# Kernel tuning notes

Hardware: AMD Instinct MI355X
Metric: run time of the kernel (lower is better)

## Reference

```python
import jax, jax.numpy as jnp
import numpy as np

B, C, T, D = 32, 1024, 64, 64
F_OUT = 128      # out_channels
S_DIM = 64       # stage_dim
N_STG = 5        # num_stages
H_MLP = 64       # hidden of stage_mlp


def setup_inputs() -> dict:
    key = jax.random.key(0)
    ks = jax.random.split(key, 16)
    sc = 0.05
    return {
        "x": jax.random.normal(ks[0], (B, C, T, D), dtype=jnp.float32),
        "A_init": jax.random.uniform(ks[1], (C, C), dtype=jnp.float32),
        "W_proj": jax.random.normal(ks[2], (F_OUT, D), dtype=jnp.float32) * sc,
        "b_proj": jnp.zeros((F_OUT,), dtype=jnp.float32),
        "W_s1": jax.random.normal(ks[3], (H_MLP, D), dtype=jnp.float32) * sc,
        "b_s1": jnp.zeros((H_MLP,), dtype=jnp.float32),
        "W_s2": jax.random.normal(ks[4], (N_STG, H_MLP), dtype=jnp.float32) * sc,
        "b_s2": jnp.zeros((N_STG,), dtype=jnp.float32),
        "W_c1": jax.random.normal(ks[5], (S_DIM, N_STG), dtype=jnp.float32) * sc,
        "b_c1": jnp.zeros((S_DIM,), dtype=jnp.float32),
        "W_c2": jax.random.normal(ks[6], (S_DIM, S_DIM), dtype=jnp.float32) * sc,
        "b_c2": jnp.zeros((S_DIM,), dtype=jnp.float32),
        "att": jax.random.normal(ks[7], (2 * F_OUT + S_DIM,), dtype=jnp.float32) * sc,
        "lam": jnp.array([0.5], dtype=jnp.float32),
    }


def reference(x, A_init, W_proj, b_proj, W_s1, b_s1, W_s2, b_s2,
              W_c1, b_c1, W_c2, b_c2, att, lam):
    F = W_proj.shape[0]
    x_red = jnp.mean(x, axis=2)                               # (B,C,D)
    Z = x_red @ W_proj.T + b_proj                             # (B,C,F)
    x_glob = jnp.mean(x_red, axis=1)                          # (B,D)
    s = jax.nn.softmax(
        jax.nn.relu(x_glob @ W_s1.T + b_s1) @ W_s2.T + b_s2, axis=-1)  # (B,num_stages)
    c = jax.nn.relu(s @ W_c1.T + b_c1) @ W_c2.T + b_c2        # (B,stage_dim)
    # Split att_weight: sum over concat([Z_i, Z_j, c]) * att == dot-per-part
    a_i, a_j, a_c = att[:F], att[F:2 * F], att[2 * F:]
    e = ((Z @ a_i)[:, :, None]            # (B,C,1) broadcast over j
         + (Z @ a_j)[:, None, :]          # (B,1,C) broadcast over i
         + (c @ a_c)[:, None, None])      # (B,1,1)
    e = jax.nn.leaky_relu(e, negative_slope=0.2)              # (B,C,C)
    eps = 1e-8
    e_tilde = e + lam[0] * jnp.log(A_init + eps)[None, :, :]
    alpha = jax.nn.softmax(e_tilde, axis=-1)                  # (B,C,C)
    h = alpha @ Z                                             # (B,C,F)
    return h, s
```

## Files before the change

kernel.cpp:

```cpp
#include <hip/hip_runtime.h>
#include <cstddef>
#include <math.h>


typedef __attribute__((ext_vector_type(8))) short bf16x8;
typedef __attribute__((ext_vector_type(4))) float f32x4;

__device__ inline unsigned f2bf(float f) {
  unsigned u = __float_as_uint(f);
  return (u + 0x7FFFu + ((u >> 16) & 1u)) >> 16;
}

#define LOGA_OFF 0u
#define EI_OFF   1048576u
#define EJ_OFF   1081344u
#define PXG_OFF  1114112u
#define ZK_OFF   1179648u

__global__ __launch_bounds__(256) void k_fuse1(
    const float4* __restrict__ X4, const float* __restrict__ A,
    const float* __restrict__ lam, const float* __restrict__ W,
    const float* __restrict__ bproj, const float* __restrict__ att,
    uint4* __restrict__ Zk, float* __restrict__ ei, float* __restrict__ ej,
    float4* __restrict__ pXG4, float* __restrict__ llogA) {
  int tid = threadIdx.x;
  int bk = blockIdx.x;
  if (bk >= 1024) {
    float l = lam[0];
    int base = (bk - 1024) * 1024 + tid;
#pragma unroll
    for (int k = 0; k < 4; ++k)
      llogA[base + k * 256] = l * __logf(A[base + k * 256] + 1e-8f);
    return;
  }
  __shared__ float Wl[64 * 129];
  __shared__ float4 xr4[32 * 16];
  int rb = bk * 32;

#pragma unroll
  for (int k = 0; k < 32; ++k) {
    int g = k * 256 + tid;
    Wl[(g & 63) * 129 + (g >> 6)] = W[g];
  }

  {
    int row = tid >> 3, g = tid & 7;
    const float4* xbase = X4 + ((size_t)(rb + row)) * 1024 + g;
    float4 a0 = make_float4(0.f, 0.f, 0.f, 0.f), a1 = a0;
#pragma unroll
    for (int k = 0; k < 128; k += 2) {
      float4 v0 = xbase[k * 8];
      float4 v1 = xbase[k * 8 + 8];
      a0.x += v0.x; a0.y += v0.y; a0.z += v0.z; a0.w += v0.w;
      a1.x += v1.x; a1.y += v1.y; a1.z += v1.z; a1.w += v1.w;
    }
    const float inv = 1.0f / 64.0f;
    a0.x *= inv; a0.y *= inv; a0.z *= inv; a0.w *= inv;
    a1.x *= inv; a1.y *= inv; a1.z *= inv; a1.w *= inv;
    xr4[row * 16 + g] = a0;
    xr4[row * 16 + g + 8] = a1;
  }
  __syncthreads();

  if (tid < 16) {
    float4 p = make_float4(0.f, 0.f, 0.f, 0.f);
#pragma unroll
    for (int r = 0; r < 32; ++r) {
      float4 v = xr4[r * 16 + tid];
      p.x += v.x; p.y += v.y; p.z += v.z; p.w += v.w;
    }
    pXG4[bk * 16 + tid] = p;
  }

  int f = tid & 127, rg = tid >> 7;
  float wreg[64];
#pragma unroll
  for (int d = 0; d < 64; ++d) wreg[d] = Wl[d * 129 + f];
  float bias = bproj[f];
  float acc[16];
#pragma unroll
  for (int r = 0; r < 16; ++r) acc[r] = bias;
#pragma unroll
  for (int r = 0; r < 16; ++r) {
    int row = rg * 16 + r;
#pragma unroll
    for (int dq = 0; dq < 16; ++dq) {
      float4 xv = xr4[row * 16 + dq];
      acc[r] = fmaf(wreg[dq * 4 + 0], xv.x, acc[r]);
      acc[r] = fmaf(wreg[dq * 4 + 1], xv.y, acc[r]);
      acc[r] = fmaf(wreg[dq * 4 + 2], xv.z, acc[r]);
      acc[r] = fmaf(wreg[dq * 4 + 3], xv.w, acc[r]);
    }
  }
  int b = rb >> 10;
  int cbase = (rb & 1023) + rg * 16;
#pragma unroll
  for (int k2 = 0; k2 < 2; ++k2) {
    unsigned w0 = f2bf(acc[k2 * 8 + 0]) | (f2bf(acc[k2 * 8 + 1]) << 16);
    unsigned w1 = f2bf(acc[k2 * 8 + 2]) | (f2bf(acc[k2 * 8 + 3]) << 16);
    unsigned w2 = f2bf(acc[k2 * 8 + 4]) | (f2bf(acc[k2 * 8 + 5]) << 16);
    unsigned w3 = f2bf(acc[k2 * 8 + 6]) | (f2bf(acc[k2 * 8 + 7]) << 16);
    size_t chunk = ((size_t)b * 128 + ((cbase >> 3) + k2)) * 128 + f;
    Zk[chunk] = make_uint4(w0, w1, w2, w3);
  }
  __syncthreads();
  float* Zl = Wl;
#pragma unroll
  for (int r = 0; r < 16; ++r)
    Zl[(rg * 16 + r) * 130 + f] = acc[r];
  __syncthreads();
  int row = tid >> 3, g = tid & 7;
  float si = 0.f, sj = 0.f;
#pragma unroll
  for (int u = 0; u < 16; ++u) {
    float z = Zl[row * 130 + g * 16 + u];
    si = fmaf(z, att[g * 16 + u], si);
    sj = fmaf(z, att[128 + g * 16 + u], sj);
  }
  si += __shfl_xor(si, 1); sj += __shfl_xor(sj, 1);
  si += __shfl_xor(si, 2); sj += __shfl_xor(sj, 2);
  si += __shfl_xor(si, 4); sj += __shfl_xor(sj, 4);
  if (g == 0) { ei[rb + row] = si; ej[rb + row] = sj; }
}

__global__ __launch_bounds__(64) void k_main(const uint4* __restrict__ Zk,
    const float* __restrict__ llogA, const float* __restrict__ ei,
    const float* __restrict__ ej, const float* __restrict__ pXG,
    const float* __restrict__ Ws1, const float* __restrict__ bs1,
    const float* __restrict__ Ws2, const float* __restrict__ bs2,
    const float* __restrict__ Wc1, const float* __restrict__ bc1,
    const float* __restrict__ Wc2, const float* __restrict__ bc2,
    const float* __restrict__ att,
    float* __restrict__ hout, float* __restrict__ sout) {
  int bid = blockIdx.x;
  int b = ((bid & 7) << 2) | ((bid >> 3) & 3);
  int rowgrp = bid >> 5;
  int i0 = rowgrp * 16;
  int lane = threadIdx.x;
  int lg = lane >> 4, ln = lane & 15;

  float ecb;
  {
    float xg = 0.f;
    const float* pb = pXG + (size_t)b * 32 * 64;
#pragma unroll 8
    for (int p = 0; p < 32; ++p) xg += pb[p * 64 + lane];
    xg *= (1.0f / 1024.0f);
    const float* w1 = Ws1 + lane * 64;
    float h = bs1[lane];
#pragma unroll 16
    for (int d = 0; d < 64; ++d) h = fmaf(__shfl(xg, d), w1[d], h);
    h = fmaxf(h, 0.f);
    int ln5 = lane < 5 ? lane : 4;
    const float* w2 = Ws2 + ln5 * 64;
    float l = bs2[ln5];
#pragma unroll 16
    for (int k = 0; k < 64; ++k) l = fmaf(__shfl(h, k), w2[k], l);
    float s0 = __shfl(l, 0), s1 = __shfl(l, 1), s2 = __shfl(l, 2),
          s3 = __shfl(l, 3), s4 = __shfl(l, 4);
    float m = fmaxf(fmaxf(fmaxf(s0, s1), fmaxf(s2, s3)), s4);
    float e0 = __expf(s0 - m), e1 = __expf(s1 - m), e2 = __expf(s2 - m),
          e3 = __expf(s3 - m), e4 = __expf(s4 - m);
    float inv = 1.0f / (e0 + e1 + e2 + e3 + e4);
    s0 = e0 * inv; s1 = e1 * inv; s2 = e2 * inv; s3 = e3 * inv; s4 = e4 * inv;
    if (rowgrp == 0 && lane == 0) {
      sout[b * 5 + 0] = s0; sout[b * 5 + 1] = s1; sout[b * 5 + 2] = s2;
      sout[b * 5 + 3] = s3; sout[b * 5 + 4] = s4;
    }
    const float* wc1 = Wc1 + lane * 5;
    float cv = bc1[lane];
    cv = fmaf(s0, wc1[0], cv); cv = fmaf(s1, wc1[1], cv);
    cv = fmaf(s2, wc1[2], cv); cv = fmaf(s3, wc1[3], cv);
    cv = fmaf(s4, wc1[4], cv);
    cv = fmaxf(cv, 0.f);
    const float* wc2 = Wc2 + lane * 64;
    float c2 = bc2[lane];
#pragma unroll 16
    for (int k = 0; k < 64; ++k) c2 = fmaf(__shfl(cv, k), wc2[k], c2);
    float v = c2 * att[256 + lane];
#pragma unroll
    for (int o = 32; o; o >>= 1) v += __shfl_xor(v, o);
    ecb = v;
  }

  int i_gl = i0 + ln;
  float eir = ei[b * 1024 + i_gl];
  const float4* lrow4 = (const float4*)(llogA + (size_t)i_gl * 1024);
  const float4* ejr4  = (const float4*)(ej + b * 1024);
  const uint4*  ZkB   = Zk + (size_t)b * 128 * 128;

  float m_run = -1e30f, s_run = 0.0f;
  f32x4 acc[8];
#pragma unroll
  for (int q = 0; q < 8; ++q) { f32x4 z = {0.f, 0.f, 0.f, 0.f}; acc[q] = z; }

  for (int jt = 0; jt < 16; ++jt) {
    int j0 = jt * 64;
    uint4 bz[2][8];
#pragma unroll
    for (int ks = 0; ks < 2; ++ks)
#pragma unroll
      for (int fb = 0; fb < 8; ++fb)
        bz[ks][fb] = ZkB[(size_t)((j0 >> 3) + ks * 4 + lg) * 128 + fb * 16 + ln];
    float tv[16];
    float tm = -1e30f;
#pragma unroll
    for (int ks = 0; ks < 2; ++ks) {
      int jb = (j0 + ks * 32 + lg * 8) >> 2;
      float4 e0 = ejr4[jb], e1 = ejr4[jb + 1];
      float4 l0 = lrow4[jb], l1 = lrow4[jb + 1];
      float eq[8] = {e0.x, e0.y, e0.z, e0.w, e1.x, e1.y, e1.z, e1.w};
      float lq[8] = {l0.x, l0.y, l0.z, l0.w, l1.x, l1.y, l1.z, l1.w};
#pragma unroll
      for (int u = 0; u < 8; ++u) {
        float t = eir + eq[u] + ecb;
        t = t > 0.0f ? t : 0.2f * t;
        t += lq[u];
        tv[ks * 8 + u] = t;
        tm = fmaxf(tm, t);
      }
    }
    tm = fmaxf(tm, __shfl_xor(tm, 16));
    tm = fmaxf(tm, __shfl_xor(tm, 32));
    float newm = fmaxf(m_run, tm);
    float scale = __expf(m_run - newm);
    float ts = 0.0f;
    unsigned pw[8];
#pragma unroll
    for (int q = 0; q < 8; ++q) {
      float p0 = __expf(tv[2 * q] - newm);
      float p1 = __expf(tv[2 * q + 1] - newm);
      ts += p0 + p1;
      pw[q] = f2bf(p0) | (f2bf(p1) << 16);
    }
    ts += __shfl_xor(ts, 16);
    ts += __shfl_xor(ts, 32);
    s_run = s_run * scale + ts;
    m_run = newm;
#pragma unroll
    for (int q = 0; q < 8; ++q) acc[q] *= scale;
    union { unsigned u[4]; bf16x8 v; } c0, c1;
#pragma unroll
    for (int q = 0; q < 4; ++q) { c0.u[q] = pw[q]; c1.u[q] = pw[4 + q]; }
#pragma unroll
    for (int fb = 0; fb < 8; ++fb)
      acc[fb] = __builtin_amdgcn_mfma_f32_16x16x32_bf16(c0.v, *(bf16x8*)&bz[0][fb], acc[fb], 0, 0, 0);
#pragma unroll
    for (int fb = 0; fb < 8; ++fb)
      acc[fb] = __builtin_amdgcn_mfma_f32_16x16x32_bf16(c1.v, *(bf16x8*)&bz[1][fb], acc[fb], 0, 0, 0);
  }

  float invs = 1.0f / s_run;
  float inv_m[4];
#pragma unroll
  for (int r = 0; r < 4; ++r) inv_m[r] = __shfl(invs, lg * 4 + r);
  float* hb = hout + ((size_t)b * 1024 + i0 + lg * 4) * 128 + ln;
#pragma unroll
  for (int fb = 0; fb < 8; ++fb) {
#pragma unroll
    for (int r = 0; r < 4; ++r)
      hb[(size_t)r * 128 + fb * 16] = acc[fb][r] * inv_m[r];
  }
}

extern "C" void kernel_launch(void* const* d_in, const int* in_sizes, int n_in,
                              void* d_out, int out_size, void* d_ws, size_t ws_size,
                              hipStream_t stream) {
  const float* x     = (const float*)d_in[0];
  const float* Ainit = (const float*)d_in[1];
  const float* Wproj = (const float*)d_in[2];
  const float* bproj = (const float*)d_in[3];
  const float* Ws1   = (const float*)d_in[4];
  const float* bs1   = (const float*)d_in[5];
  const float* Ws2   = (const float*)d_in[6];
  const float* bs2   = (const float*)d_in[7];
  const float* Wc1   = (const float*)d_in[8];
  const float* bc1   = (const float*)d_in[9];
  const float* Wc2   = (const float*)d_in[10];
  const float* bc2   = (const float*)d_in[11];
  const float* att   = (const float*)d_in[12];
  const float* lam   = (const float*)d_in[13];

  float* ws    = (float*)d_ws;
  float* llogA = ws + LOGA_OFF;
  float* ei    = ws + EI_OFF;
  float* ej    = ws + EJ_OFF;
  float* pXG   = ws + PXG_OFF;
  uint4* Zk    = (uint4*)(ws + ZK_OFF);

  float* hout = (float*)d_out;
  float* sout = hout + (size_t)32 * 1024 * 128;

  hipLaunchKernelGGL(k_fuse1, dim3(2048), dim3(256), 0, stream,
                     (const float4*)x, Ainit, lam, Wproj, bproj, att,
                     Zk, ei, ej, (float4*)pXG, llogA);
  hipLaunchKernelGGL(k_main,  dim3(2048), dim3(64),  0, stream,
                     Zk, llogA, ei, ej, pXG,
                     Ws1, bs1, Ws2, bs2, Wc1, bc1, Wc2, bc2, att,
                     hout, sout);
}
```

Before: 180.6 us.

## Split k_main feature columns across waves, share stage MLP, skip redundant rescale

k_main now runs 256-thread blocks in which four waves cover two row groups, each wave handling half of the 128 output features. The stage MLP is computed once per block by wave 0 and shared through shared memory, so it is no longer repeated in every 64-thread block. The online softmax skips rescaling the accumulators when the running max does not change. k_fuse1 reads projection weights straight from global memory as float4 instead of transposing them through shared memory, which removes a barrier. In exchange, the per-row softmax exp work is now duplicated across the two feature-half waves, and the kernel adds a block barrier plus a divergent branch.

Result: slower. 207.4 us (+14.9%).

```diff
diff --git a/kernel.cpp b/kernel.cpp
--- a/kernel.cpp
+++ b/kernel.cpp
@@ -33,15 +33,9 @@
       llogA[base + k * 256] = l * __logf(A[base + k * 256] + 1e-8f);
     return;
   }
-  __shared__ float Wl[64 * 129];
   __shared__ float4 xr4[32 * 16];
+  __shared__ float Zl[32 * 130];
   int rb = bk * 32;
-
-#pragma unroll
-  for (int k = 0; k < 32; ++k) {
-    int g = k * 256 + tid;
-    Wl[(g & 63) * 129 + (g >> 6)] = W[g];
-  }
 
   {
     int row = tid >> 3, g = tid & 7;
@@ -74,8 +68,15 @@
 
   int f = tid & 127, rg = tid >> 7;
   float wreg[64];
-#pragma unroll
-  for (int d = 0; d < 64; ++d) wreg[d] = Wl[d * 129 + f];
+  {
+    const float4* Wf = (const float4*)(W + f * 64);
+#pragma unroll
+    for (int q = 0; q < 16; ++q) {
+      float4 w = Wf[q];
+      wreg[q * 4 + 0] = w.x; wreg[q * 4 + 1] = w.y;
+      wreg[q * 4 + 2] = w.z; wreg[q * 4 + 3] = w.w;
+    }
+  }
   float bias = bproj[f];
   float acc[16];
 #pragma unroll
@@ -103,8 +104,6 @@
     size_t chunk = ((size_t)b * 128 + ((cbase >> 3) + k2)) * 128 + f;
     Zk[chunk] = make_uint4(w0, w1, w2, w3);
   }
-  __syncthreads();
-  float* Zl = Wl;
 #pragma unroll
   for (int r = 0; r < 16; ++r)
     Zl[(rg * 16 + r) * 130 + f] = acc[r];
@@ -123,7 +122,7 @@
   if (g == 0) { ei[rb + row] = si; ej[rb + row] = sj; }
 }
 
-__global__ __launch_bounds__(64) void k_main(const uint4* __restrict__ Zk,
+__global__ __launch_bounds__(256) void k_main(const uint4* __restrict__ Zk,
     const float* __restrict__ llogA, const float* __restrict__ ei,
     const float* __restrict__ ej, const float* __restrict__ pXG,
     const float* __restrict__ Ws1, const float* __restrict__ bs1,
@@ -132,15 +131,18 @@
     const float* __restrict__ Wc2, const float* __restrict__ bc2,
     const float* __restrict__ att,
     float* __restrict__ hout, float* __restrict__ sout) {
+  __shared__ float ec_s;
   int bid = blockIdx.x;
   int b = ((bid & 7) << 2) | ((bid >> 3) & 3);
-  int rowgrp = bid >> 5;
+  int rgpair = bid >> 5;
+  int tid = threadIdx.x;
+  int wave = tid >> 6, lane = tid & 63;
+  int rowgrp = rgpair * 2 + (wave >> 1);
+  int fbase = (wave & 1) * 4;
   int i0 = rowgrp * 16;
-  int lane = threadIdx.x;
   int lg = lane >> 4, ln = lane & 15;
 
-  float ecb;
-  {
+  if (wave == 0) {
     float xg = 0.f;
     const float* pb = pXG + (size_t)b * 32 * 64;
 #pragma unroll 8
@@ -163,7 +165,7 @@
           e3 = __expf(s3 - m), e4 = __expf(s4 - m);
     float inv = 1.0f / (e0 + e1 + e2 + e3 + e4);
     s0 = e0 * inv; s1 = e1 * inv; s2 = e2 * inv; s3 = e3 * inv; s4 = e4 * inv;
-    if (rowgrp == 0 && lane == 0) {
+    if (rgpair == 0 && lane == 0) {
       sout[b * 5 + 0] = s0; sout[b * 5 + 1] = s1; sout[b * 5 + 2] = s2;
       sout[b * 5 + 3] = s3; sout[b * 5 + 4] = s4;
     }
@@ -180,8 +182,10 @@
     float v = c2 * att[256 + lane];
 #pragma unroll
     for (int o = 32; o; o >>= 1) v += __shfl_xor(v, o);
-    ecb = v;
-  }
+    if (lane == 0) ec_s = v;
+  }
+  __syncthreads();
+  float ecb = ec_s;
 
   int i_gl = i0 + ln;
   float eir = ei[b * 1024 + i_gl];
@@ -190,18 +194,19 @@
   const uint4*  ZkB   = Zk + (size_t)b * 128 * 128;
 
   float m_run = -1e30f, s_run = 0.0f;
-  f32x4 acc[8];
-#pragma unroll
-  for (int q = 0; q < 8; ++q) { f32x4 z = {0.f, 0.f, 0.f, 0.f}; acc[q] = z; }
+  f32x4 acc[4];
+#pragma unroll
+  for (int q = 0; q < 4; ++q) { f32x4 z = {0.f, 0.f, 0.f, 0.f}; acc[q] = z; }
 
   for (int jt = 0; jt < 16; ++jt) {
     int j0 = jt * 64;
-    uint4 bz[2][8];
+    uint4 bz[2][4];
 #pragma unroll
     for (int ks = 0; ks < 2; ++ks)
 #pragma unroll
-      for (int fb = 0; fb < 8; ++fb)
-        bz[ks][fb] = ZkB[(size_t)((j0 >> 3) + ks * 4 + lg) * 128 + fb * 16 + ln];
+      for (int fb = 0; fb < 4; ++fb)
+        bz[ks][fb] = ZkB[(size_t)((j0 >> 3) + ks * 4 + lg) * 128
+                         + (fbase + fb) * 16 + ln];
     float tv[16];
     float tm = -1e30f;
 #pragma unroll
@@ -223,30 +228,33 @@
     tm = fmaxf(tm, __shfl_xor(tm, 16));
     tm = fmaxf(tm, __shfl_xor(tm, 32));
     float newm = fmaxf(m_run, tm);
-    float scale = __expf(m_run - newm);
+    if (!__all(tm <= m_run)) {
+      float scale = __expf(m_run - newm);
+      s_run *= scale;
+#pragma unroll
+      for (int q = 0; q < 4; ++q) acc[q] *= scale;
+      m_run = newm;
+    }
     float ts = 0.0f;
     unsigned pw[8];
 #pragma unroll
     for (int q = 0; q < 8; ++q) {
-      float p0 = __expf(tv[2 * q] - newm);
-      float p1 = __expf(tv[2 * q + 1] - newm);
+      float p0 = __expf(tv[2 * q] - m_run);
+      float p1 = __expf(tv[2 * q + 1] - m_run);
       ts += p0 + p1;
       pw[q] = f2bf(p0) | (f2bf(p1) << 16);
     }
     ts += __shfl_xor(ts, 16);
     ts += __shfl_xor(ts, 32);
-    s_run = s_run * scale + ts;
-    m_run = newm;
-#pragma unroll
-    for (int q = 0; q < 8; ++q) acc[q] *= scale;
+    s_run += ts;
     union { unsigned u[4]; bf16x8 v; } c0, c1;
 #pragma unroll
     for (int q = 0; q < 4; ++q) { c0.u[q] = pw[q]; c1.u[q] = pw[4 + q]; }
 #pragma unroll
-    for (int fb = 0; fb < 8; ++fb)
+    for (int fb = 0; fb < 4; ++fb)
       acc[fb] = __builtin_amdgcn_mfma_f32_16x16x32_bf16(c0.v, *(bf16x8*)&bz[0][fb], acc[fb], 0, 0, 0);
 #pragma unroll
-    for (int fb = 0; fb < 8; ++fb)
+    for (int fb = 0; fb < 4; ++fb)
       acc[fb] = __builtin_amdgcn_mfma_f32_16x16x32_bf16(c1.v, *(bf16x8*)&bz[1][fb], acc[fb], 0, 0, 0);
   }
 
@@ -254,9 +262,9 @@
   float inv_m[4];
 #pragma unroll
   for (int r = 0; r < 4; ++r) inv_m[r] = __shfl(invs, lg * 4 + r);
-  float* hb = hout + ((size_t)b * 1024 + i0 + lg * 4) * 128 + ln;
-#pragma unroll
-  for (int fb = 0; fb < 8; ++fb) {
+  float* hb = hout + ((size_t)b * 1024 + i0 + lg * 4) * 128 + fbase * 16 + ln;
+#pragma unroll
+  for (int fb = 0; fb < 4; ++fb) {
 #pragma unroll
     for (int r = 0; r < 4; ++r)
       hb[(size_t)r * 128 + fb * 16] = acc[fb][r] * inv_m[r];
@@ -294,7 +302,7 @@
   hipLaunchKernelGGL(k_fuse1, dim3(2048), dim3(256), 0, stream,
                      (const float4*)x, Ainit, lam, Wproj, bproj, att,
                      Zk, ei, ej, (float4*)pXG, llogA);
-  hipLaunchKernelGGL(k_main,  dim3(2048), dim3(64),  0, stream,
+  hipLaunchKernelGGL(k_main,  dim3(1024), dim3(256), 0, stream,
                      Zk, llogA, ei, ej, pXG,
                      Ws1, bs1, Ws2, bs2, Wc1, bc1, Wc2, bc2, att,
                      hout, sout);
```

## Double-buffer Z and logA tile loads and stage ej in shared memory

Applied to the files above, without the earlier changes.

The main attention kernel's j-tile loop now prefetches the next tile's Z fragments and logA row values into a second register buffer while the current tile is processed. This lets global-load latency overlap the softmax and MFMA work. The per-batch ej vector is also copied into LDS once at kernel start instead of being read from global memory every tile. The cost is roughly double the register footprint for the Z buffers, which may reduce occupancy or cause spills, plus one extra barrier.

New measurement: 183.7 us. No clear change (+1.8%).

```diff
diff --git a/kernel.cpp b/kernel.cpp
--- a/kernel.cpp
+++ b/kernel.cpp
@@ -132,12 +132,18 @@
     const float* __restrict__ Wc2, const float* __restrict__ bc2,
     const float* __restrict__ att,
     float* __restrict__ hout, float* __restrict__ sout) {
+  __shared__ float4 ejs4[256];
   int bid = blockIdx.x;
   int b = ((bid & 7) << 2) | ((bid >> 3) & 3);
   int rowgrp = bid >> 5;
   int i0 = rowgrp * 16;
   int lane = threadIdx.x;
   int lg = lane >> 4, ln = lane & 15;
+
+  const float4* ej4 = (const float4*)(ej + b * 1024);
+#pragma unroll
+  for (int k = 0; k < 4; ++k) ejs4[k * 64 + lane] = ej4[k * 64 + lane];
+  __syncthreads();
 
   float ecb;
   {
@@ -186,7 +192,6 @@
   int i_gl = i0 + ln;
   float eir = ei[b * 1024 + i_gl];
   const float4* lrow4 = (const float4*)(llogA + (size_t)i_gl * 1024);
-  const float4* ejr4  = (const float4*)(ej + b * 1024);
   const uint4*  ZkB   = Zk + (size_t)b * 128 * 128;
 
   float m_run = -1e30f, s_run = 0.0f;
@@ -194,61 +199,72 @@
 #pragma unroll
   for (int q = 0; q < 8; ++q) { f32x4 z = {0.f, 0.f, 0.f, 0.f}; acc[q] = z; }
 
-  for (int jt = 0; jt < 16; ++jt) {
-    int j0 = jt * 64;
-    uint4 bz[2][8];
-#pragma unroll
-    for (int ks = 0; ks < 2; ++ks)
-#pragma unroll
-      for (int fb = 0; fb < 8; ++fb)
-        bz[ks][fb] = ZkB[(size_t)((j0 >> 3) + ks * 4 + lg) * 128 + fb * 16 + ln];
-    float tv[16];
-    float tm = -1e30f;
-#pragma unroll
-    for (int ks = 0; ks < 2; ++ks) {
-      int jb = (j0 + ks * 32 + lg * 8) >> 2;
-      float4 e0 = ejr4[jb], e1 = ejr4[jb + 1];
-      float4 l0 = lrow4[jb], l1 = lrow4[jb + 1];
-      float eq[8] = {e0.x, e0.y, e0.z, e0.w, e1.x, e1.y, e1.z, e1.w};
-      float lq[8] = {l0.x, l0.y, l0.z, l0.w, l1.x, l1.y, l1.z, l1.w};
-#pragma unroll
-      for (int u = 0; u < 8; ++u) {
-        float t = eir + eq[u] + ecb;
-        t = t > 0.0f ? t : 0.2f * t;
-        t += lq[u];
-        tv[ks * 8 + u] = t;
-        tm = fmaxf(tm, t);
-      }
-    }
-    tm = fmaxf(tm, __shfl_xor(tm, 16));
-    tm = fmaxf(tm, __shfl_xor(tm, 32));
-    float newm = fmaxf(m_run, tm);
-    float scale = __expf(m_run - newm);
-    float ts = 0.0f;
-    unsigned pw[8];
-#pragma unroll
-    for (int q = 0; q < 8; ++q) {
-      float p0 = __expf(tv[2 * q] - newm);
-      float p1 = __expf(tv[2 * q + 1] - newm);
-      ts += p0 + p1;
-      pw[q] = f2bf(p0) | (f2bf(p1) << 16);
-    }
-    ts += __shfl_xor(ts, 16);
-    ts += __shfl_xor(ts, 32);
-    s_run = s_run * scale + ts;
-    m_run = newm;
-#pragma unroll
-    for (int q = 0; q < 8; ++q) acc[q] *= scale;
-    union { unsigned u[4]; bf16x8 v; } c0, c1;
-#pragma unroll
-    for (int q = 0; q < 4; ++q) { c0.u[q] = pw[q]; c1.u[q] = pw[4 + q]; }
-#pragma unroll
-    for (int fb = 0; fb < 8; ++fb)
-      acc[fb] = __builtin_amdgcn_mfma_f32_16x16x32_bf16(c0.v, *(bf16x8*)&bz[0][fb], acc[fb], 0, 0, 0);
-#pragma unroll
-    for (int fb = 0; fb < 8; ++fb)
-      acc[fb] = __builtin_amdgcn_mfma_f32_16x16x32_bf16(c1.v, *(bf16x8*)&bz[1][fb], acc[fb], 0, 0, 0);
-  }
+#define LOAD_BZ(buf, jt_) do { int j0_ = (jt_) * 64;                          \
+  _Pragma("unroll") for (int ks = 0; ks < 2; ++ks)                            \
+    _Pragma("unroll") for (int fb = 0; fb < 8; ++fb)                          \
+      buf[ks][fb] = ZkB[(size_t)((j0_ >> 3) + ks * 4 + lg) * 128              \
+                        + fb * 16 + ln];                                      \
+} while (0)
+
+#define LOAD_LA(buf, jt_) do { int j0_ = (jt_) * 64;                          \
+  _Pragma("unroll") for (int ks = 0; ks < 2; ++ks) {                          \
+    int jb = (j0_ + ks * 32 + lg * 8) >> 2;                                   \
+    buf[ks][0] = lrow4[jb]; buf[ks][1] = lrow4[jb + 1]; }                     \
+} while (0)
+
+#define PROCESS(jt_, bz, la) do { int j0_ = (jt_) * 64;                       \
+  float tv[16]; float tm = -1e30f;                                            \
+  _Pragma("unroll") for (int ks = 0; ks < 2; ++ks) {                          \
+    int jb = (j0_ + ks * 32 + lg * 8) >> 2;                                   \
+    float4 e0 = ejs4[jb], e1 = ejs4[jb + 1];                                  \
+    float4 l0 = la[ks][0], l1 = la[ks][1];                                    \
+    float eq[8] = {e0.x, e0.y, e0.z, e0.w, e1.x, e1.y, e1.z, e1.w};           \
+    float lq[8] = {l0.x, l0.y, l0.z, l0.w, l1.x, l1.y, l1.z, l1.w};           \
+    _Pragma("unroll") for (int u = 0; u < 8; ++u) {                           \
+      float t = eir + eq[u] + ecb;                                            \
+      t = t > 0.0f ? t : 0.2f * t;                                            \
+      t += lq[u];                                                             \
+      tv[ks * 8 + u] = t; tm = fmaxf(tm, t); } }                              \
+  tm = fmaxf(tm, __shfl_xor(tm, 16));                                         \
+  tm = fmaxf(tm, __shfl_xor(tm, 32));                                         \
+  float newm = fmaxf(m_run, tm);                                              \
+  float scale = __expf(m_run - newm);                                         \
+  float ts = 0.0f; unsigned pw[8];                                            \
+  _Pragma("unroll") for (int q = 0; q < 8; ++q) {                             \
+    float p0 = __expf(tv[2 * q] - newm);                                      \
+    float p1 = __expf(tv[2 * q + 1] - newm);                                  \
+    ts += p0 + p1; pw[q] = f2bf(p0) | (f2bf(p1) << 16); }                     \
+  ts += __shfl_xor(ts, 16); ts += __shfl_xor(ts, 32);                         \
+  s_run = s_run * scale + ts; m_run = newm;                                   \
+  _Pragma("unroll") for (int q = 0; q < 8; ++q) acc[q] *= scale;              \
+  union { unsigned u[4]; bf16x8 v; } c0, c1;                                  \
+  _Pragma("unroll") for (int q = 0; q < 4; ++q) {                             \
+    c0.u[q] = pw[q]; c1.u[q] = pw[4 + q]; }                                   \
+  _Pragma("unroll") for (int fb = 0; fb < 8; ++fb)                            \
+    acc[fb] = __builtin_amdgcn_mfma_f32_16x16x32_bf16(                        \
+        c0.v, *(bf16x8*)&bz[0][fb], acc[fb], 0, 0, 0);                        \
+  _Pragma("unroll") for (int fb = 0; fb < 8; ++fb)                            \
+    acc[fb] = __builtin_amdgcn_mfma_f32_16x16x32_bf16(                        \
+        c1.v, *(bf16x8*)&bz[1][fb], acc[fb], 0, 0, 0);                        \
+} while (0)
+
+  uint4 bzA[2][8], bzB[2][8];
+  float4 laA[2][2], laB[2][2];
+  LOAD_BZ(bzA, 0);
+  LOAD_LA(laA, 0);
+  for (int jt = 0; jt < 16; jt += 2) {
+    LOAD_BZ(bzB, jt + 1);
+    LOAD_LA(laB, jt + 1);
+    PROCESS(jt, bzA, laA);
+    if (jt + 2 < 16) {
+      LOAD_BZ(bzA, jt + 2);
+      LOAD_LA(laA, jt + 2);
+    }
+    PROCESS(jt + 1, bzB, laB);
+  }
+#undef LOAD_BZ
+#undef LOAD_LA
+#undef PROCESS
 
   float invs = 1.0f / s_run;
   float inv_m[4];
```

## Split stage MLP into own kernel and halve feature columns per attention block

Applied to the files above, without the earlier changes.

Moves the per-batch stage MLP and softmax, previously recomputed by every attention block, into a small separate kernel that writes the scalar c·a_c term to workspace. The main attention kernel now launches twice as many single-wave blocks, each covering half of the 128 output features. This reduces register pressure and raises occupancy (launch bounds 64,4), and the second Z tile load is moved after the logit computation. It also adds s_setprio around the MFMA block. The cost is that each block recomputes the exp/softmax statistics for its rows twice and there is an extra kernel launch.

New measurement: 196.3 us. 1.09x slower.

```diff
diff --git a/kernel.cpp b/kernel.cpp
--- a/kernel.cpp
+++ b/kernel.cpp
@@ -16,6 +16,7 @@
 #define EJ_OFF   1081344u
 #define PXG_OFF  1114112u
 #define ZK_OFF   1179648u
+#define EC_OFF   3276800u
 
 __global__ __launch_bounds__(256) void k_fuse1(
     const float4* __restrict__ X4, const float* __restrict__ A,
@@ -123,85 +124,88 @@
   if (g == 0) { ei[rb + row] = si; ej[rb + row] = sj; }
 }
 
-__global__ __launch_bounds__(64) void k_main(const uint4* __restrict__ Zk,
-    const float* __restrict__ llogA, const float* __restrict__ ei,
-    const float* __restrict__ ej, const float* __restrict__ pXG,
+__global__ __launch_bounds__(64) void k_ec(const float* __restrict__ pXG,
     const float* __restrict__ Ws1, const float* __restrict__ bs1,
     const float* __restrict__ Ws2, const float* __restrict__ bs2,
     const float* __restrict__ Wc1, const float* __restrict__ bc1,
     const float* __restrict__ Wc2, const float* __restrict__ bc2,
     const float* __restrict__ att,
-    float* __restrict__ hout, float* __restrict__ sout) {
+    float* __restrict__ sout, float* __restrict__ ec) {
+  int b = blockIdx.x;
+  int lane = threadIdx.x;
+  float xg = 0.f;
+  const float* pb = pXG + (size_t)b * 32 * 64;
+#pragma unroll 8
+  for (int p = 0; p < 32; ++p) xg += pb[p * 64 + lane];
+  xg *= (1.0f / 1024.0f);
+  const float* w1 = Ws1 + lane * 64;
+  float h = bs1[lane];
+#pragma unroll 16
+  for (int d = 0; d < 64; ++d) h = fmaf(__shfl(xg, d), w1[d], h);
+  h = fmaxf(h, 0.f);
+  int ln5 = lane < 5 ? lane : 4;
+  const float* w2 = Ws2 + ln5 * 64;
+  float l = bs2[ln5];
+#pragma unroll 16
+  for (int k = 0; k < 64; ++k) l = fmaf(__shfl(h, k), w2[k], l);
+  float s0 = __shfl(l, 0), s1 = __shfl(l, 1), s2 = __shfl(l, 2),
+        s3 = __shfl(l, 3), s4 = __shfl(l, 4);
+  float m = fmaxf(fmaxf(fmaxf(s0, s1), fmaxf(s2, s3)), s4);
+  float e0 = __expf(s0 - m), e1 = __expf(s1 - m), e2 = __expf(s2 - m),
+        e3 = __expf(s3 - m), e4 = __expf(s4 - m);
+  float inv = 1.0f / (e0 + e1 + e2 + e3 + e4);
+  s0 = e0 * inv; s1 = e1 * inv; s2 = e2 * inv; s3 = e3 * inv; s4 = e4 * inv;
+  if (lane == 0) {
+    sout[b * 5 + 0] = s0; sout[b * 5 + 1] = s1; sout[b * 5 + 2] = s2;
+    sout[b * 5 + 3] = s3; sout[b * 5 + 4] = s4;
+  }
+  const float* wc1 = Wc1 + lane * 5;
+  float cv = bc1[lane];
+  cv = fmaf(s0, wc1[0], cv); cv = fmaf(s1, wc1[1], cv);
+  cv = fmaf(s2, wc1[2], cv); cv = fmaf(s3, wc1[3], cv);
+  cv = fmaf(s4, wc1[4], cv);
+  cv = fmaxf(cv, 0.f);
+  const float* wc2 = Wc2 + lane * 64;
+  float c2 = bc2[lane];
+#pragma unroll 16
+  for (int k = 0; k < 64; ++k) c2 = fmaf(__shfl(cv, k), wc2[k], c2);
+  float v = c2 * att[256 + lane];
+#pragma unroll
+  for (int o = 32; o; o >>= 1) v += __shfl_xor(v, o);
+  if (lane == 0) ec[b] = v;
+}
+
+__global__ __launch_bounds__(64, 4) void k_main(const uint4* __restrict__ Zk,
+    const float* __restrict__ llogA, const float* __restrict__ ei,
+    const float* __restrict__ ej, const float* __restrict__ ecw,
+    float* __restrict__ hout) {
   int bid = blockIdx.x;
   int b = ((bid & 7) << 2) | ((bid >> 3) & 3);
-  int rowgrp = bid >> 5;
+  int r = bid >> 5;
+  int rowgrp = r >> 1;
+  int fbase = (r & 1) * 4;
   int i0 = rowgrp * 16;
   int lane = threadIdx.x;
   int lg = lane >> 4, ln = lane & 15;
 
-  float ecb;
-  {
-    float xg = 0.f;
-    const float* pb = pXG + (size_t)b * 32 * 64;
-#pragma unroll 8
-    for (int p = 0; p < 32; ++p) xg += pb[p * 64 + lane];
-    xg *= (1.0f / 1024.0f);
-    const float* w1 = Ws1 + lane * 64;
-    float h = bs1[lane];
-#pragma unroll 16
-    for (int d = 0; d < 64; ++d) h = fmaf(__shfl(xg, d), w1[d], h);
-    h = fmaxf(h, 0.f);
-    int ln5 = lane < 5 ? lane : 4;
-    const float* w2 = Ws2 + ln5 * 64;
-    float l = bs2[ln5];
-#pragma unroll 16
-    for (int k = 0; k < 64; ++k) l = fmaf(__shfl(h, k), w2[k], l);
-    float s0 = __shfl(l, 0), s1 = __shfl(l, 1), s2 = __shfl(l, 2),
-          s3 = __shfl(l, 3), s4 = __shfl(l, 4);
-    float m = fmaxf(fmaxf(fmaxf(s0, s1), fmaxf(s2, s3)), s4);
-    float e0 = __expf(s0 - m), e1 = __expf(s1 - m), e2 = __expf(s2 - m),
-          e3 = __expf(s3 - m), e4 = __expf(s4 - m);
-    float inv = 1.0f / (e0 + e1 + e2 + e3 + e4);
-    s0 = e0 * inv; s1 = e1 * inv; s2 = e2 * inv; s3 = e3 * inv; s4 = e4 * inv;
-    if (rowgrp == 0 && lane == 0) {
-      sout[b * 5 + 0] = s0; sout[b * 5 + 1] = s1; sout[b * 5 + 2] = s2;
-      sout[b * 5 + 3] = s3; sout[b * 5 + 4] = s4;
-    }
-    const float* wc1 = Wc1 + lane * 5;
-    float cv = bc1[lane];
-    cv = fmaf(s0, wc1[0], cv); cv = fmaf(s1, wc1[1], cv);
-    cv = fmaf(s2, wc1[2], cv); cv = fmaf(s3, wc1[3], cv);
-    cv = fmaf(s4, wc1[4], cv);
-    cv = fmaxf(cv, 0.f);
-    const float* wc2 = Wc2 + lane * 64;
-    float c2 = bc2[lane];
-#pragma unroll 16
-    for (int k = 0; k < 64; ++k) c2 = fmaf(__shfl(cv, k), wc2[k], c2);
-    float v = c2 * att[256 + lane];
-#pragma unroll
-    for (int o = 32; o; o >>= 1) v += __shfl_xor(v, o);
-    ecb = v;
-  }
-
   int i_gl = i0 + ln;
   float eir = ei[b * 1024 + i_gl];
+  float ecb = ecw[b];
   const float4* lrow4 = (const float4*)(llogA + (size_t)i_gl * 1024);
   const float4* ejr4  = (const float4*)(ej + b * 1024);
   const uint4*  ZkB   = Zk + (size_t)b * 128 * 128;
 
   float m_run = -1e30f, s_run = 0.0f;
-  f32x4 acc[8];
-#pragma unroll
-  for (int q = 0; q < 8; ++q) { f32x4 z = {0.f, 0.f, 0.f, 0.f}; acc[q] = z; }
+  f32x4 acc[4];
+#pragma unroll
+  for (int q = 0; q < 4; ++q) { f32x4 z = {0.f, 0.f, 0.f, 0.f}; acc[q] = z; }
 
   for (int jt = 0; jt < 16; ++jt) {
     int j0 = jt * 64;
-    uint4 bz[2][8];
-#pragma unroll
-    for (int ks = 0; ks < 2; ++ks)
-#pragma unroll
-      for (int fb = 0; fb < 8; ++fb)
-        bz[ks][fb] = ZkB[(size_t)((j0 >> 3) + ks * 4 + lg) * 128 + fb * 16 + ln];
+    uint4 bz0[4];
+#pragma unroll
+    for (int fb = 0; fb < 4; ++fb)
+      bz0[fb] = ZkB[(size_t)((j0 >> 3) + lg) * 128 + (fbase + fb) * 16 + ln];
     float tv[16];
     float tm = -1e30f;
 #pragma unroll
@@ -220,6 +224,10 @@
         tm = fmaxf(tm, t);
       }
     }
+    uint4 bz1[4];
+#pragma unroll
+    for (int fb = 0; fb < 4; ++fb)
+      bz1[fb] = ZkB[(size_t)((j0 >> 3) + 4 + lg) * 128 + (fbase + fb) * 16 + ln];
     tm = fmaxf(tm, __shfl_xor(tm, 16));
     tm = fmaxf(tm, __shfl_xor(tm, 32));
     float newm = fmaxf(m_run, tm);
@@ -238,28 +246,30 @@
     s_run = s_run * scale + ts;
     m_run = newm;
 #pragma unroll
-    for (int q = 0; q < 8; ++q) acc[q] *= scale;
+    for (int q = 0; q < 4; ++q) acc[q] *= scale;
     union { unsigned u[4]; bf16x8 v; } c0, c1;
 #pragma unroll
     for (int q = 0; q < 4; ++q) { c0.u[q] = pw[q]; c1.u[q] = pw[4 + q]; }
-#pragma unroll
-    for (int fb = 0; fb < 8; ++fb)
-      acc[fb] = __builtin_amdgcn_mfma_f32_16x16x32_bf16(c0.v, *(bf16x8*)&bz[0][fb], acc[fb], 0, 0, 0);
-#pragma unroll
-    for (int fb = 0; fb < 8; ++fb)
-      acc[fb] = __builtin_amdgcn_mfma_f32_16x16x32_bf16(c1.v, *(bf16x8*)&bz[1][fb], acc[fb], 0, 0, 0);
+    __builtin_amdgcn_s_setprio(1);
+#pragma unroll
+    for (int fb = 0; fb < 4; ++fb)
+      acc[fb] = __builtin_amdgcn_mfma_f32_16x16x32_bf16(c0.v, *(bf16x8*)&bz0[fb], acc[fb], 0, 0, 0);
+#pragma unroll
+    for (int fb = 0; fb < 4; ++fb)
+      acc[fb] = __builtin_amdgcn_mfma_f32_16x16x32_bf16(c1.v, *(bf16x8*)&bz1[fb], acc[fb], 0, 0, 0);
+    __builtin_amdgcn_s_setprio(0);
   }
 
   float invs = 1.0f / s_run;
   float inv_m[4];
 #pragma unroll
-  for (int r = 0; r < 4; ++r) inv_m[r] = __shfl(invs, lg * 4 + r);
-  float* hb = hout + ((size_t)b * 1024 + i0 + lg * 4) * 128 + ln;
-#pragma unroll
-  for (int fb = 0; fb < 8; ++fb) {
-#pragma unroll
-    for (int r = 0; r < 4; ++r)
-      hb[(size_t)r * 128 + fb * 16] = acc[fb][r] * inv_m[r];
+  for (int rr = 0; rr < 4; ++rr) inv_m[rr] = __shfl(invs, lg * 4 + rr);
+  float* hb = hout + ((size_t)b * 1024 + i0 + lg * 4) * 128 + fbase * 16 + ln;
+#pragma unroll
+  for (int fb = 0; fb < 4; ++fb) {
+#pragma unroll
+    for (int rr = 0; rr < 4; ++rr)
+      hb[(size_t)rr * 128 + fb * 16] = acc[fb][rr] * inv_m[rr];
   }
 }
 
@@ -287,6 +297,7 @@
   float* ej    = ws + EJ_OFF;
   float* pXG   = ws + PXG_OFF;
   uint4* Zk    = (uint4*)(ws + ZK_OFF);
+  float* ec    = ws + EC_OFF;
 
   float* hout = (float*)d_out;
   float* sout = hout + (size_t)32 * 1024 * 128;
@@ -294,8 +305,9 @@
   hipLaunchKernelGGL(k_fuse1, dim3(2048), dim3(256), 0, stream,
                      (const float4*)x, Ainit, lam, Wproj, bproj, att,
                      Zk, ei, ej, (float4*)pXG, llogA);
-  hipLaunchKernelGGL(k_main,  dim3(2048), dim3(64),  0, stream,
-                     Zk, llogA, ei, ej, pXG,
+  hipLaunchKernelGGL(k_ec,    dim3(32),   dim3(64),  0, stream, pXG,
                      Ws1, bs1, Ws2, bs2, Wc1, bc1, Wc2, bc2, att,
-                     hout, sout);
-}
+                     sout, ec);
+  hipLaunchKernelGGL(k_main,  dim3(4096), dim3(64),  0, stream,
+                     Zk, llogA, ei, ej, ec, hout);
+}
```
